# Optimization experiments

Hardware: AMD Instinct MI355X
Metric: run time of the kernel (lower is better)

The kernel has to match this reference:

```python
import jax, jax.numpy as jnp
import numpy as np

N, E, F_IN, H1, H2, C = 100000, 800000, 182, 128, 64, 2


def setup_inputs() -> dict:
    key = jax.random.key(0)
    ks = jax.random.split(key, 10)
    s = 0.05
    return {
        "x": jax.random.normal(ks[0], (N, F_IN), dtype=jnp.float32),
        "edge_index": jax.random.randint(ks[1], (2, E), 0, N, dtype=jnp.int32),
        "W1_l": jax.random.normal(ks[2], (H1, F_IN), dtype=jnp.float32) * s,
        "W1_r": jax.random.normal(ks[3], (H1, F_IN), dtype=jnp.float32) * s,
        "b1": jnp.zeros((H1,), dtype=jnp.float32),
        "W2_l": jax.random.normal(ks[4], (H2, H1), dtype=jnp.float32) * s,
        "W2_r": jax.random.normal(ks[5], (H2, H1), dtype=jnp.float32) * s,
        "b2": jnp.zeros((H2,), dtype=jnp.float32),
        "W_lin": jax.random.normal(ks[6], (C, H2), dtype=jnp.float32) * s,
        "b_lin": jnp.zeros((C,), dtype=jnp.float32),
    }


def _sage_conv(x, src, dst, Wl, Wr, b):
    # mean-aggregate neighbor messages x[src] onto dst, then two linears
    msg = x[src]                                            # [E, F]
    ssum = jax.ops.segment_sum(msg, dst, num_segments=N)    # [N, F]
    cnt = jax.ops.segment_sum(jnp.ones((src.shape[0], 1), x.dtype), dst, num_segments=N)
    mean = ssum / jnp.maximum(cnt, 1.0)                     # [N, F]
    return mean @ Wl.T + x @ Wr.T + b                       # [N, F_out]


def reference(x, edge_index, W1_l, W1_r, b1, W2_l, W2_r, b2, W_lin, b_lin):
    src, dst = edge_index[0], edge_index[1]
    h = jax.nn.relu(_sage_conv(x, src, dst, W1_l, W1_r, b1))   # dropout is identity in eval
    h = jax.nn.relu(_sage_conv(h, src, dst, W2_l, W2_r, b2))
    logits = h @ W_lin.T + b_lin
    return jax.nn.log_softmax(logits, axis=1)
```

## Files before the change

### kernel.cpp

```cpp
#include <hip/hip_runtime.h>
#include <math.h>

#define F_IN 182
#define H1   128
#define H2   64

typedef short bf16x8 __attribute__((ext_vector_type(8)));
typedef float f32x4 __attribute__((ext_vector_type(4)));

__device__ __forceinline__ float b2f(short s) {
    unsigned u = ((unsigned)(unsigned short)s) << 16;
    return __builtin_bit_cast(float, u);
}
__device__ __forceinline__ short f2b(float f) {
    unsigned u = __builtin_bit_cast(unsigned, f);
    unsigned r = (u + 0x7FFFu + ((u >> 16) & 1u)) >> 16;
    return (short)(unsigned short)r;
}

#define GLOAD16(g, l) __builtin_amdgcn_global_load_lds( \
    (const __attribute__((address_space(1))) void*)(g), \
    (__attribute__((address_space(3))) void*)(l), 16, 0, 0)

__global__ __launch_bounds__(256) void prelude(
    int* __restrict__ cnt, int Nn, int zB,
    const float* __restrict__ W1l, const float* __restrict__ W1r, short* __restrict__ wc1,
    const float* __restrict__ W2l, const float* __restrict__ W2r, short* __restrict__ wc2)
{
    int b = blockIdx.x, tid = threadIdx.x;
    if (b < zB) {
        int i = (b * 256 + tid) * 4;
        if (i + 4 <= Nn) {
            int4 z = make_int4(0, 0, 0, 0);
            *(int4*)(cnt + i) = z;
        } else {
            for (int j = i; j < Nn; ++j) cnt[j] = 0;
        }
        return;
    }
    b -= zB;
    if (b < 192) {
        int idx = b * 256 + tid;
        int r = idx / 192, k = idx - r * 192;
        float v = 0.f;
        if (k < F_IN) v = (r < 128) ? W1l[r * F_IN + k] : W1r[(r - 128) * F_IN + k];
        wc1[idx] = f2b(v);
        return;
    }
    b -= 192;
    {
        int idx = b * 256 + tid;
        int r = idx >> 7, k = idx & 127;
        float v = (r < 64) ? W2l[r * 128 + k] : W2r[(r - 64) * 128 + k];
        wc2[idx] = f2b(v);
    }
}

__global__ __launch_bounds__(256) void scan_block(const int* __restrict__ in,
                                                  int* __restrict__ out,
                                                  int* __restrict__ bsums, int Nn) {
    __shared__ int s[256];
    int b = blockIdx.x, t = threadIdx.x;
    int base = b * 2048 + t * 8;
    int v[8]; int sum = 0;
#pragma unroll
    for (int i = 0; i < 8; ++i) { int idx = base + i; v[i] = (idx < Nn) ? in[idx] : 0; sum += v[i]; }
    s[t] = sum; __syncthreads();
    for (int off = 1; off < 256; off <<= 1) {
        int x = (t >= off) ? s[t - off] : 0; __syncthreads();
        s[t] += x; __syncthreads();
    }
    int excl = s[t] - sum;
    if (t == 255) bsums[b] = s[255];
    int run = excl;
#pragma unroll
    for (int i = 0; i < 8; ++i) { int idx = base + i; if (idx < Nn) out[idx] = run; run += v[i]; }
}

__global__ __launch_bounds__(64) void scan_bsums(int* bs, int nb) {
    int l = threadIdx.x;
    int v = (l < nb) ? bs[l] : 0;
    int s = v;
#pragma unroll
    for (int off = 1; off < 64; off <<= 1) {
        int t = __shfl_up(s, off, 64);
        if (l >= off) s += t;
    }
    if (l < nb) bs[l] = s - v;
}

__global__ __launch_bounds__(256) void scan_add(int* __restrict__ offs,
                                                const int* __restrict__ bs, int Nn) {
    int i = blockIdx.x * 256 + threadIdx.x;
    if (i < Nn) offs[i] += bs[i >> 11];
}

__global__ __launch_bounds__(256) void csr_scatter(const int* __restrict__ srcv,
                                                   const int* __restrict__ dstv,
                                                   const int* __restrict__ rank,
                                                   const int* __restrict__ offs,
                                                   int* __restrict__ csr, int E) {
    int base = (blockIdx.x * 256 + threadIdx.x) * 4;
    if (base + 4 <= E) {
        int4 d = *(const int4*)(dstv + base);
        int4 s = *(const int4*)(srcv + base);
        int4 rk = *(const int4*)(rank + base);
        csr[offs[d.x] + rk.x] = s.x;
        csr[offs[d.y] + rk.y] = s.y;
        csr[offs[d.z] + rk.z] = s.z;
        csr[offs[d.w] + rk.w] = s.w;
    } else {
        for (int e = base; e < E; ++e) csr[offs[dstv[e]] + rank[e]] = srcv[e];
    }
}

template <int NC, int KK, int KREAL, bool AF32, bool DEG>
__global__ __launch_bounds__(512) void gemm_fused(
    const void* __restrict__ Ap, const short* __restrict__ Wcat,
    short* __restrict__ outL, short* __restrict__ outR, int M,
    const int* __restrict__ dstv, int* __restrict__ cnt, int* __restrict__ rank,
    int E, int degB)
{
    constexpr int BM = 128, BK = 64;
    constexpr int WN = NC / 4;
    constexpr int NJ = WN / 16;
    constexpr int CB = NC * 8 / 512;
    __shared__ __attribute__((aligned(16))) short sA[BM * BK];
    __shared__ __attribute__((aligned(16))) short sB[NC * BK];
    int tid = threadIdx.x;

    if (DEG && (int)blockIdx.x < degB) {
        int base = ((int)blockIdx.x * 512 + tid) * 4;
        if (base + 4 <= E) {
            int4 d = *(const int4*)(dstv + base);
            int4 rk;
            rk.x = atomicAdd(&cnt[d.x], 1);
            rk.y = atomicAdd(&cnt[d.y], 1);
            rk.z = atomicAdd(&cnt[d.z], 1);
            rk.w = atomicAdd(&cnt[d.w], 1);
            *(int4*)(rank + base) = rk;
        } else {
            for (int e = base; e < E; ++e) rank[e] = atomicAdd(&cnt[dstv[e]], 1);
        }
        return;
    }
    int bx = DEG ? ((int)blockIdx.x - degB) : (int)blockIdx.x;
    int wid = tid >> 6, lane = tid & 63;
    int wr = wid >> 2, wc = wid & 3;
    int row0 = bx * BM;
    bool full = (row0 + BM <= M);
    f32x4 acc[4][NJ] = {};
#pragma unroll
    for (int ksi = 0; ksi < KK / BK; ++ksi) {
        const int k0 = ksi * BK;
        if (AF32) {
            const float* Af = (const float*)Ap;
#pragma unroll
            for (int it = 0; it < 2; ++it) {
                int i = it * 512 + tid;
                int r = i >> 3, oct = i & 7;
                int gr = row0 + r;
                int gk = k0 + oct * 8;
                bf16x8 v = {};
                if (gr < M) {
                    const float* p = Af + (size_t)gr * KREAL + gk;
                    if (k0 + BK <= KREAL) {
                        float2 f0 = *(const float2*)(p + 0);
                        float2 f1 = *(const float2*)(p + 2);
                        float2 f2 = *(const float2*)(p + 4);
                        float2 f3 = *(const float2*)(p + 6);
                        v[0] = f2b(f0.x); v[1] = f2b(f0.y);
                        v[2] = f2b(f1.x); v[3] = f2b(f1.y);
                        v[4] = f2b(f2.x); v[5] = f2b(f2.y);
                        v[6] = f2b(f3.x); v[7] = f2b(f3.y);
                    } else {
#pragma unroll
                        for (int j = 0; j < 4; ++j) {
                            if (gk + 2 * j + 2 <= KREAL) {
                                float2 f = *(const float2*)(p + 2 * j);
                                v[2 * j] = f2b(f.x); v[2 * j + 1] = f2b(f.y);
                            }
                        }
                    }
                }
                *(bf16x8*)((char*)sA + r * 128 + ((oct * 16) ^ ((r & 7) << 4))) = v;
            }
        } else {
            const char* Ab = (const char*)Ap;
            if (full) {
#pragma unroll
                for (int c = 0; c < 2; ++c) {
                    int idx = (wid * 2 + c) * 64 + lane;
                    int r = idx >> 3, cs = (idx & 7) * 16;
                    const char* g = Ab + (size_t)(row0 + r) * (KK * 2) + k0 * 2 + (cs ^ ((r & 7) << 4));
                    GLOAD16(g, (char*)sA + (size_t)(wid * 2 + c) * 1024);
                }
            } else {
                for (int t = tid; t < BM * 8; t += 512) {
                    int r = t >> 3, kc = (t & 7) * 16;
                    bf16x8 v = {};
                    int gr = row0 + r;
                    if (gr < M) v = *(const bf16x8*)(Ab + (size_t)gr * (KK * 2) + k0 * 2 + kc);
                    *(bf16x8*)((char*)sA + r * 128 + (kc ^ ((r & 7) << 4))) = v;
                }
            }
        }
#pragma unroll
        for (int c = 0; c < CB; ++c) {
            int idx = (wid * CB + c) * 64 + lane;
            int r = idx >> 3, cs = (idx & 7) * 16;
            const char* g = (const char*)Wcat + (size_t)r * (KK * 2) + k0 * 2 + (cs ^ ((r & 7) << 4));
            GLOAD16(g, (char*)sB + (size_t)(wid * CB + c) * 1024);
        }
        __syncthreads();
        int rl = lane & 15;
        int sw = (rl & 7) << 4;
#pragma unroll
        for (int ks = 0; ks < 2; ++ks) {
            int kb2 = ks * 64 + (lane >> 4) * 16;
            int cswz = kb2 ^ sw;
            bf16x8 af[4];
#pragma unroll
            for (int mi = 0; mi < 4; ++mi) {
                int row = wr * 64 + mi * 16 + rl;
                af[mi] = *(const bf16x8*)((const char*)sA + row * 128 + cswz);
            }
#pragma unroll
            for (int ni = 0; ni < NJ; ++ni) {
                int rowb = wc * WN + ni * 16 + rl;
                bf16x8 bfr = *(const bf16x8*)((const char*)sB + rowb * 128 + cswz);
#pragma unroll
                for (int mi = 0; mi < 4; ++mi)
                    acc[mi][ni] = __builtin_amdgcn_mfma_f32_16x16x32_bf16(af[mi], bfr, acc[mi][ni], 0, 0, 0);
            }
        }
        __syncthreads();
    }
    constexpr int HN = NC / 2;
#pragma unroll
    for (int mi = 0; mi < 4; ++mi) {
#pragma unroll
        for (int ni = 0; ni < NJ; ++ni) {
            int gc = wc * WN + ni * 16 + (lane & 15);
#pragma unroll
            for (int r = 0; r < 4; ++r) {
                int gr = row0 + wr * 64 + mi * 16 + (lane >> 4) * 4 + r;
                if (gr < M) {
                    short v = f2b(acc[mi][ni][r]);
                    if (gc < HN) outL[(size_t)gr * HN + gc] = v;
                    else         outR[(size_t)gr * HN + gc - HN] = v;
                }
            }
        }
    }
}

__global__ __launch_bounds__(256) void agg_fuse1(const int* __restrict__ offs,
                                                 const int* __restrict__ degs,
                                                 const int* __restrict__ csr,
                                                 const short* __restrict__ yl,
                                                 const short* __restrict__ yr,
                                                 const float* __restrict__ bias,
                                                 short* __restrict__ h, int Nn) {
    int gid = blockIdx.x * 16 + (threadIdx.x >> 4);
    int l = threadIdx.x & 15;
    if (gid >= Nn) return;
    int start = offs[gid], deg = degs[gid];
    const int co = l * 8;
    float a[8] = {};
    int t = 0;
    for (; t + 4 <= deg; t += 4) {
        int s0 = csr[start + t], s1 = csr[start + t + 1];
        int s2 = csr[start + t + 2], s3 = csr[start + t + 3];
        bf16x8 v0 = *(const bf16x8*)(yl + (size_t)s0 * H1 + co);
        bf16x8 v1 = *(const bf16x8*)(yl + (size_t)s1 * H1 + co);
        bf16x8 v2 = *(const bf16x8*)(yl + (size_t)s2 * H1 + co);
        bf16x8 v3 = *(const bf16x8*)(yl + (size_t)s3 * H1 + co);
#pragma unroll
        for (int j = 0; j < 8; ++j)
            a[j] += b2f(v0[j]) + b2f(v1[j]) + b2f(v2[j]) + b2f(v3[j]);
    }
    for (; t < deg; ++t) {
        int s = csr[start + t];
        bf16x8 v = *(const bf16x8*)(yl + (size_t)s * H1 + co);
#pragma unroll
        for (int j = 0; j < 8; ++j) a[j] += b2f(v[j]);
    }
    float inv = 1.f / fmaxf((float)deg, 1.f);
    bf16x8 rv = *(const bf16x8*)(yr + (size_t)gid * H1 + co);
    bf16x8 o;
#pragma unroll
    for (int j = 0; j < 8; ++j)
        o[j] = f2b(fmaxf(a[j] * inv + b2f(rv[j]) + bias[co + j], 0.f));
    *(bf16x8*)(h + (size_t)gid * H1 + co) = o;
}

__global__ __launch_bounds__(256) void agg_head2(const int* __restrict__ offs,
                                                 const int* __restrict__ degs,
                                                 const int* __restrict__ csr,
                                                 const short* __restrict__ yl,
                                                 const short* __restrict__ yr,
                                                 const float* __restrict__ bias,
                                                 const float* __restrict__ Wlin,
                                                 const float* __restrict__ blin,
                                                 float* __restrict__ out, int Nn) {
    int gid = blockIdx.x * 16 + (threadIdx.x >> 4);
    int l = threadIdx.x & 15;
    if (gid >= Nn) return;
    int start = offs[gid], deg = degs[gid];
    const int co = l * 4;
    float a[4] = {};
    int t = 0;
    for (; t + 4 <= deg; t += 4) {
        int s0 = csr[start + t], s1 = csr[start + t + 1];
        int s2 = csr[start + t + 2], s3 = csr[start + t + 3];
        short4 v0 = *(const short4*)(yl + (size_t)s0 * H2 + co);
        short4 v1 = *(const short4*)(yl + (size_t)s1 * H2 + co);
        short4 v2 = *(const short4*)(yl + (size_t)s2 * H2 + co);
        short4 v3 = *(const short4*)(yl + (size_t)s3 * H2 + co);
        a[0] += b2f(v0.x) + b2f(v1.x) + b2f(v2.x) + b2f(v3.x);
        a[1] += b2f(v0.y) + b2f(v1.y) + b2f(v2.y) + b2f(v3.y);
        a[2] += b2f(v0.z) + b2f(v1.z) + b2f(v2.z) + b2f(v3.z);
        a[3] += b2f(v0.w) + b2f(v1.w) + b2f(v2.w) + b2f(v3.w);
    }
    for (; t < deg; ++t) {
        int s = csr[start + t];
        short4 v = *(const short4*)(yl + (size_t)s * H2 + co);
        a[0] += b2f(v.x); a[1] += b2f(v.y); a[2] += b2f(v.z); a[3] += b2f(v.w);
    }
    float inv = 1.f / fmaxf((float)deg, 1.f);
    short4 rv = *(const short4*)(yr + (size_t)gid * H2 + co);
    float h0 = fmaxf(a[0] * inv + b2f(rv.x) + bias[co + 0], 0.f);
    float h1v = fmaxf(a[1] * inv + b2f(rv.y) + bias[co + 1], 0.f);
    float h2v = fmaxf(a[2] * inv + b2f(rv.z) + bias[co + 2], 0.f);
    float h3v = fmaxf(a[3] * inv + b2f(rv.w) + bias[co + 3], 0.f);
    float g0 = h0 * Wlin[co] + h1v * Wlin[co + 1] + h2v * Wlin[co + 2] + h3v * Wlin[co + 3];
    float g1 = h0 * Wlin[64 + co] + h1v * Wlin[64 + co + 1] + h2v * Wlin[64 + co + 2] + h3v * Wlin[64 + co + 3];
#pragma unroll
    for (int m = 8; m >= 1; m >>= 1) {
        g0 += __shfl_xor(g0, m, 16);
        g1 += __shfl_xor(g1, m, 16);
    }
    if (l == 0) {
        g0 += blin[0]; g1 += blin[1];
        float mx = fmaxf(g0, g1);
        float lse = mx + logf(expf(g0 - mx) + expf(g1 - mx));
        float2 r; r.x = g0 - lse; r.y = g1 - lse;
        ((float2*)out)[gid] = r;
    }
}

extern "C" void kernel_launch(void* const* d_in, const int* in_sizes, int n_in,
                              void* d_out, int out_size, void* d_ws, size_t ws_size,
                              hipStream_t stream) {
    const float* x    = (const float*)d_in[0];
    const int*   ei   = (const int*)d_in[1];
    const float* W1l  = (const float*)d_in[2];
    const float* W1r  = (const float*)d_in[3];
    const float* b1   = (const float*)d_in[4];
    const float* W2l  = (const float*)d_in[5];
    const float* W2r  = (const float*)d_in[6];
    const float* b2   = (const float*)d_in[7];
    const float* Wlin = (const float*)d_in[8];
    const float* blin = (const float*)d_in[9];
    float* outp = (float*)d_out;

    const int N = in_sizes[0] / F_IN;
    const int E = in_sizes[1] / 2;
    const int* srcv = ei;
    const int* dstv = ei + E;

    char* ws = (char*)d_ws;
    size_t o = 0;
    auto alloc = [&](size_t bytes) { size_t r = o; o += (bytes + 255) & ~(size_t)255; return r; };
    int* cnt_i  = (int*)(ws + alloc((size_t)N * 4));
    int* offs   = (int*)(ws + alloc((size_t)N * 4));
    int* bsums  = (int*)(ws + alloc(1024));
    int* rank   = (int*)(ws + alloc((size_t)E * 4));
    int* csr    = (int*)(ws + alloc((size_t)E * 4));
    short* wc1  = (short*)(ws + alloc((size_t)256 * 192 * 2));
    short* wc2  = (short*)(ws + alloc((size_t)128 * 128 * 2));
    short* y1l  = (short*)(ws + alloc((size_t)N * H1 * 2));
    short* y1r  = (short*)(ws + alloc((size_t)N * H1 * 2));
    short* h1   = (short*)(ws + alloc((size_t)N * H1 * 2));
    short* y2l  = y1l;
    short* y2r  = y1r;

    const int zB   = (N + 1023) / 1024;
    const int degB = (E + 2047) / 2048;
    const int nb   = (N + 2047) / 2048;
    const int nthr = (N + 255) / 256;
    const int gblk = (N + 127) / 128;
    const int e4   = (E + 1023) / 1024;
    const int a16  = (N + 15) / 16;

    prelude<<<zB + 192 + 64, 256, 0, stream>>>(cnt_i, N, zB, W1l, W1r, wc1, W2l, W2r, wc2);

    gemm_fused<256, 192, F_IN, true, true><<<degB + gblk, 512, 0, stream>>>(
        x, wc1, y1l, y1r, N, dstv, cnt_i, rank, E, degB);

    scan_block<<<nb, 256, 0, stream>>>(cnt_i, offs, bsums, N);
    scan_bsums<<<1, 64, 0, stream>>>(bsums, nb);
    scan_add<<<nthr, 256, 0, stream>>>(offs, bsums, N);

    csr_scatter<<<e4, 256, 0, stream>>>(srcv, dstv, rank, offs, csr, E);

    agg_fuse1<<<a16, 256, 0, stream>>>(offs, cnt_i, csr, y1l, y1r, b1, h1, N);

    gemm_fused<128, 128, 128, false, false><<<gblk, 512, 0, stream>>>(
        h1, wc2, y2l, y2r, N, nullptr, nullptr, nullptr, 0, 0);

    agg_head2<<<a16, 256, 0, stream>>>(offs, cnt_i, csr, y2l, y2r, b2, Wlin, blin, outp, N);
}
```

Baseline: 171.2 us.

## Fold block-sum scan into scan_add, unroll gathers by 8, use library bf16 convert

Removes the separate single-block scan_bsums launch: every scan_add block now rescans the 64 block sums in one wavefront and keeps them in shared memory. Both aggregation kernels gain an 8-wide gather loop that issues eight neighbor loads before summing, to expose more memory-level parallelism. The hand-written round-to-nearest-even float-to-bf16 conversion is replaced with the HIP library intrinsic, possibly enabling packed hardware conversion. Register pressure rises in the aggregation kernels, and every scan_add block repeats the small scan.

```diff
diff --git a/kernel.cpp b/kernel.cpp
--- a/kernel.cpp
+++ b/kernel.cpp
@@ -1,4 +1,5 @@
 #include <hip/hip_runtime.h>
+#include <hip/hip_bf16.h>
 #include <math.h>
 
 #define F_IN 182
@@ -13,9 +14,13 @@
     return __builtin_bit_cast(float, u);
 }
 __device__ __forceinline__ short f2b(float f) {
-    unsigned u = __builtin_bit_cast(unsigned, f);
-    unsigned r = (u + 0x7FFFu + ((u >> 16) & 1u)) >> 16;
-    return (short)(unsigned short)r;
+    return __builtin_bit_cast(short, __float2bfloat16(f));
+}
+__device__ __forceinline__ short2 f2x2(float2 f) {
+    short2 r;
+    r.x = f2b(f.x);
+    r.y = f2b(f.y);
+    return r;
 }
 
 #define GLOAD16(g, l) __builtin_amdgcn_global_load_lds( \
@@ -77,22 +82,24 @@
     for (int i = 0; i < 8; ++i) { int idx = base + i; if (idx < Nn) out[idx] = run; run += v[i]; }
 }
 
-__global__ __launch_bounds__(64) void scan_bsums(int* bs, int nb) {
-    int l = threadIdx.x;
-    int v = (l < nb) ? bs[l] : 0;
-    int s = v;
-#pragma unroll
-    for (int off = 1; off < 64; off <<= 1) {
-        int t = __shfl_up(s, off, 64);
-        if (l >= off) s += t;
-    }
-    if (l < nb) bs[l] = s - v;
-}
-
 __global__ __launch_bounds__(256) void scan_add(int* __restrict__ offs,
-                                                const int* __restrict__ bs, int Nn) {
-    int i = blockIdx.x * 256 + threadIdx.x;
-    if (i < Nn) offs[i] += bs[i >> 11];
+                                                const int* __restrict__ bsums,
+                                                int nb, int Nn) {
+    __shared__ int sbs[64];
+    int t = threadIdx.x;
+    if (t < 64) {
+        int v = (t < nb) ? bsums[t] : 0;
+        int s = v;
+#pragma unroll
+        for (int off = 1; off < 64; off <<= 1) {
+            int u = __shfl_up(s, off, 64);
+            if (t >= off) s += u;
+        }
+        sbs[t] = s - v;
+    }
+    __syncthreads();
+    int i = blockIdx.x * 256 + t;
+    if (i < Nn) offs[i] += sbs[i >> 11];
 }
 
 __global__ __launch_bounds__(256) void csr_scatter(const int* __restrict__ srcv,
@@ -169,16 +176,15 @@
                         float2 f1 = *(const float2*)(p + 2);
                         float2 f2 = *(const float2*)(p + 4);
                         float2 f3 = *(const float2*)(p + 6);
-                        v[0] = f2b(f0.x); v[1] = f2b(f0.y);
-                        v[2] = f2b(f1.x); v[3] = f2b(f1.y);
-                        v[4] = f2b(f2.x); v[5] = f2b(f2.y);
-                        v[6] = f2b(f3.x); v[7] = f2b(f3.y);
+                        short2 p0 = f2x2(f0), p1 = f2x2(f1), p2 = f2x2(f2), p3 = f2x2(f3);
+                        v[0] = p0.x; v[1] = p0.y; v[2] = p1.x; v[3] = p1.y;
+                        v[4] = p2.x; v[5] = p2.y; v[6] = p3.x; v[7] = p3.y;
                     } else {
 #pragma unroll
                         for (int j = 0; j < 4; ++j) {
                             if (gk + 2 * j + 2 <= KREAL) {
-                                float2 f = *(const float2*)(p + 2 * j);
-                                v[2 * j] = f2b(f.x); v[2 * j + 1] = f2b(f.y);
+                                short2 pj = f2x2(*(const float2*)(p + 2 * j));
+                                v[2 * j] = pj.x; v[2 * j + 1] = pj.y;
                             }
                         }
                     }
@@ -269,13 +275,28 @@
     const int co = l * 8;
     float a[8] = {};
     int t = 0;
+    for (; t + 8 <= deg; t += 8) {
+        int idx[8];
+#pragma unroll
+        for (int q = 0; q < 8; ++q) idx[q] = csr[start + t + q];
+        bf16x8 vv[8];
+#pragma unroll
+        for (int q = 0; q < 8; ++q) vv[q] = *(const bf16x8*)(yl + (size_t)idx[q] * H1 + co);
+#pragma unroll
+        for (int j = 0; j < 8; ++j) {
+            float s = 0.f;
+#pragma unroll
+            for (int q = 0; q < 8; ++q) s += b2f(vv[q][j]);
+            a[j] += s;
+        }
+    }
     for (; t + 4 <= deg; t += 4) {
-        int s0 = csr[start + t], s1 = csr[start + t + 1];
-        int s2 = csr[start + t + 2], s3 = csr[start + t + 3];
-        bf16x8 v0 = *(const bf16x8*)(yl + (size_t)s0 * H1 + co);
-        bf16x8 v1 = *(const bf16x8*)(yl + (size_t)s1 * H1 + co);
-        bf16x8 v2 = *(const bf16x8*)(yl + (size_t)s2 * H1 + co);
-        bf16x8 v3 = *(const bf16x8*)(yl + (size_t)s3 * H1 + co);
+        int i0 = csr[start + t], i1 = csr[start + t + 1];
+        int i2 = csr[start + t + 2], i3 = csr[start + t + 3];
+        bf16x8 v0 = *(const bf16x8*)(yl + (size_t)i0 * H1 + co);
+        bf16x8 v1 = *(const bf16x8*)(yl + (size_t)i1 * H1 + co);
+        bf16x8 v2 = *(const bf16x8*)(yl + (size_t)i2 * H1 + co);
+        bf16x8 v3 = *(const bf16x8*)(yl + (size_t)i3 * H1 + co);
 #pragma unroll
         for (int j = 0; j < 8; ++j)
             a[j] += b2f(v0[j]) + b2f(v1[j]) + b2f(v2[j]) + b2f(v3[j]);
@@ -290,8 +311,11 @@
     bf16x8 rv = *(const bf16x8*)(yr + (size_t)gid * H1 + co);
     bf16x8 o;
 #pragma unroll
-    for (int j = 0; j < 8; ++j)
-        o[j] = f2b(fmaxf(a[j] * inv + b2f(rv[j]) + bias[co + j], 0.f));
+    for (int j = 0; j < 4; ++j) {
+        float r0 = fmaxf(a[2 * j] * inv + b2f(rv[2 * j]) + bias[co + 2 * j], 0.f);
+        float r1 = fmaxf(a[2 * j + 1] * inv + b2f(rv[2 * j + 1]) + bias[co + 2 * j + 1], 0.f);
+        o[2 * j] = f2b(r0); o[2 * j + 1] = f2b(r1);
+    }
     *(bf16x8*)(h + (size_t)gid * H1 + co) = o;
 }
 
@@ -311,13 +335,26 @@
     const int co = l * 4;
     float a[4] = {};
     int t = 0;
+    for (; t + 8 <= deg; t += 8) {
+        int idx[8];
+#pragma unroll
+        for (int q = 0; q < 8; ++q) idx[q] = csr[start + t + q];
+        short4 vv[8];
+#pragma unroll
+        for (int q = 0; q < 8; ++q) vv[q] = *(const short4*)(yl + (size_t)idx[q] * H2 + co);
+#pragma unroll
+        for (int q = 0; q < 8; ++q) {
+            a[0] += b2f(vv[q].x); a[1] += b2f(vv[q].y);
+            a[2] += b2f(vv[q].z); a[3] += b2f(vv[q].w);
+        }
+    }
     for (; t + 4 <= deg; t += 4) {
-        int s0 = csr[start + t], s1 = csr[start + t + 1];
-        int s2 = csr[start + t + 2], s3 = csr[start + t + 3];
-        short4 v0 = *(const short4*)(yl + (size_t)s0 * H2 + co);
-        short4 v1 = *(const short4*)(yl + (size_t)s1 * H2 + co);
-        short4 v2 = *(const short4*)(yl + (size_t)s2 * H2 + co);
-        short4 v3 = *(const short4*)(yl + (size_t)s3 * H2 + co);
+        int i0 = csr[start + t], i1 = csr[start + t + 1];
+        int i2 = csr[start + t + 2], i3 = csr[start + t + 3];
+        short4 v0 = *(const short4*)(yl + (size_t)i0 * H2 + co);
+        short4 v1 = *(const short4*)(yl + (size_t)i1 * H2 + co);
+        short4 v2 = *(const short4*)(yl + (size_t)i2 * H2 + co);
+        short4 v3 = *(const short4*)(yl + (size_t)i3 * H2 + co);
         a[0] += b2f(v0.x) + b2f(v1.x) + b2f(v2.x) + b2f(v3.x);
         a[1] += b2f(v0.y) + b2f(v1.y) + b2f(v2.y) + b2f(v3.y);
         a[2] += b2f(v0.z) + b2f(v1.z) + b2f(v2.z) + b2f(v3.z);
@@ -400,8 +437,7 @@
         x, wc1, y1l, y1r, N, dstv, cnt_i, rank, E, degB);
 
     scan_block<<<nb, 256, 0, stream>>>(cnt_i, offs, bsums, N);
-    scan_bsums<<<1, 64, 0, stream>>>(bsums, nb);
-    scan_add<<<nthr, 256, 0, stream>>>(offs, bsums, N);
+    scan_add<<<nthr, 256, 0, stream>>>(offs, bsums, nb, N);
 
     csr_scatter<<<e4, 256, 0, stream>>>(srcv, dstv, rank, offs, csr, E);
 
```

Measured after the change: 169.6 us. About the same (-0.9%).
